# Performance work log

Measured on AMD Instinct MI355X. Metric: run time of the kernel, lower is better.

Reference implementation:

```python
import jax, jax.numpy as jnp
import numpy as np

N, E, IN_CH, EDGE_DIM, N_GRAPHS = 8000, 64000, 256, 16, 64
HEADS = (3, 2, 2, 1)
OUT_CH = (512, 512, 256, 256)
IN_CHS = (IN_CH, 1536, 1024, 512)
NEG_SLOPE = 0.2  # PyG GATv2Conv default negative_slope


def setup_inputs() -> dict:
    key = jax.random.key(0)
    ks = iter(jax.random.split(key, 64))
    d = {}
    d["x"] = jax.random.normal(next(ks), (N, IN_CH), jnp.float32)
    d["edge_index"] = jax.random.randint(next(ks), (2, E), 0, N, dtype=jnp.int32)
    d["edge_attr"] = jax.random.normal(next(ks), (E, EDGE_DIM), jnp.float32)
    d["batch"] = jnp.sort(jax.random.randint(next(ks), (N,), 0, N_GRAPHS, dtype=jnp.int32))
    for i, (ci, h, co) in enumerate(zip(IN_CHS, HEADS, OUT_CH), 1):
        hc = h * co
        s = 1.0 / np.sqrt(ci)
        d[f"W{i}l"] = (jax.random.normal(next(ks), (ci, hc)) * s).astype(jnp.float32)
        d[f"b{i}l"] = jnp.zeros((hc,), jnp.float32)
        d[f"W{i}r"] = (jax.random.normal(next(ks), (ci, hc)) * s).astype(jnp.float32)
        d[f"b{i}r"] = jnp.zeros((hc,), jnp.float32)
        d[f"W{i}e"] = (jax.random.normal(next(ks), (EDGE_DIM, hc)) / np.sqrt(EDGE_DIM)).astype(jnp.float32)
        d[f"att{i}"] = (jax.random.normal(next(ks), (h, co)) / np.sqrt(co)).astype(jnp.float32)
        d[f"bias{i}"] = jnp.zeros((hc,), jnp.float32)
    d["fc1_w"] = (jax.random.normal(next(ks), (256, 64)) / 16.0).astype(jnp.float32)
    d["fc1_b"] = jnp.zeros((64,), jnp.float32)
    d["fc2_w"] = (jax.random.normal(next(ks), (64, 1)) / 8.0).astype(jnp.float32)
    d["fc2_b"] = jnp.zeros((1,), jnp.float32)
    return d


def gatv2(x, src, dst, ea, Wl, bl, Wr, br, We, att, bias, heads, co):
    """GATv2Conv forward (PyG semantics, self-loops already appended in src/dst/ea)."""
    n = x.shape[0]
    xl = (x @ Wl + bl).reshape(n, heads, co)  # applied to source nodes
    xr = (x @ Wr + br).reshape(n, heads, co)  # applied to target nodes
    ee = (ea @ We).reshape(-1, heads, co)     # edge embedding (no bias in PyG)
    m = xl[src] + xr[dst] + ee                # [E', H, C]
    logits = jnp.einsum('ehc,hc->eh', jax.nn.leaky_relu(m, NEG_SLOPE), att)
    # segmented softmax over incoming edges per destination node
    lmax = jax.ops.segment_max(logits, dst, num_segments=n)
    p = jnp.exp(logits - lmax[dst])
    denom = jax.ops.segment_sum(p, dst, num_segments=n)
    alpha = p / denom[dst]                    # every node has a self-loop -> denom > 0
    out = jax.ops.segment_sum(alpha[:, :, None] * xl[src], dst, num_segments=n)
    return out.reshape(n, heads * co) + bias


def _forward(x, edge_index, edge_attr, batch, params, fc):
    n = x.shape[0]
    src0, dst0 = edge_index[0], edge_index[1]
    # add_self_loops with fill_value='mean': per-destination mean of incoming edge_attr
    ea_sum = jax.ops.segment_sum(edge_attr, dst0, num_segments=n)
    ea_cnt = jax.ops.segment_sum(jnp.ones((edge_attr.shape[0], 1), edge_attr.dtype), dst0, num_segments=n)
    ea_loop = ea_sum / jnp.maximum(ea_cnt, 1.0)
    loop = jnp.arange(n, dtype=edge_index.dtype)
    src = jnp.concatenate([src0, loop])
    dst = jnp.concatenate([dst0, loop])
    ea = jnp.concatenate([edge_attr, ea_loop])
    h = x
    for p, hds, co in zip(params, HEADS, OUT_CH):
        h = jax.nn.relu(gatv2(h, src, dst, ea, *p, hds, co))
    # global mean pool over graphs
    s = jax.ops.segment_sum(h, batch, num_segments=N_GRAPHS)
    cnt = jax.ops.segment_sum(jnp.ones((n, 1), h.dtype), batch, num_segments=N_GRAPHS)
    g = s / jnp.maximum(cnt, 1.0)
    # dropout is identity in eval mode
    fc1_w, fc1_b, fc2_w, fc2_b = fc
    g = jax.nn.relu(g @ fc1_w + fc1_b)
    return g @ fc2_w + fc2_b


def reference(x, edge_index, edge_attr, batch,
              W1l, b1l, W1r, b1r, W1e, att1, bias1,
              W2l, b2l, W2r, b2r, W2e, att2, bias2,
              W3l, b3l, W3r, b3r, W3e, att3, bias3,
              W4l, b4l, W4r, b4r, W4e, att4, bias4,
              fc1_w, fc1_b, fc2_w, fc2_b):
    params = [(W1l, b1l, W1r, b1r, W1e, att1, bias1),
              (W2l, b2l, W2r, b2r, W2e, att2, bias2),
              (W3l, b3l, W3r, b3r, W3e, att3, bias3),
              (W4l, b4l, W4r, b4r, W4e, att4, bias4)]
    return _forward(x, edge_index, edge_attr, batch, params, (fc1_w, fc1_b, fc2_w, fc2_b))
```

## Files before the change

### kernel.cpp

```cpp
#include <hip/hip_runtime.h>
#include <math.h>

#define N_NODES 8000
#define N_EDGES 64000
#define ETOT    (N_EDGES + N_NODES)
#define EDIM    16
#define NGRAPHS 64

typedef __attribute__((ext_vector_type(8))) short short8v;
typedef __attribute__((ext_vector_type(4))) short short4v;
typedef __attribute__((ext_vector_type(4))) float f32x4;

__device__ inline unsigned short f2bf(float f) {
    unsigned u = __builtin_bit_cast(unsigned, f);
    unsigned r = (u + 0x7FFF + ((u >> 16) & 1)) >> 16;
    return (unsigned short)r;
}
__device__ inline float bf2f(unsigned short b) {
    unsigned u = ((unsigned)b) << 16;
    return __builtin_bit_cast(float, u);
}

__device__ inline void gload16(const void* g, void* l) {
    __builtin_amdgcn_global_load_lds(
        (const __attribute__((address_space(1))) void*)g,
        (__attribute__((address_space(3))) void*)l, 16, 0, 0);
}


__global__ void count_deg(const int* __restrict__ dst0, int* __restrict__ deg) {
    int e = blockIdx.x * 256 + threadIdx.x;
    if (e < N_EDGES) atomicAdd(&deg[dst0[e]], 1);
}

__global__ void scan_deg2(const int* __restrict__ deg, int* __restrict__ rowptr,
                          int* __restrict__ woff) {
    __shared__ int stot[256];
    int t = threadIdx.x;
    int base = t * 32;
    int sum = 0;
    for (int j = 0; j < 32; j++) {
        int i = base + j;
        if (i < N_NODES) sum += deg[i] + 1;
    }
    stot[t] = sum;
    __syncthreads();
    for (int off = 1; off < 256; off <<= 1) {
        int u = (t >= off) ? stot[t - off] : 0;
        __syncthreads();
        stot[t] += u;
        __syncthreads();
    }
    int run = (t == 0) ? 0 : stot[t - 1];
    if (t == 0) rowptr[0] = 0;
    for (int j = 0; j < 32; j++) {
        int i = base + j;
        if (i < N_NODES) {
            int v = deg[i] + 1;
            woff[i] = run;
            rowptr[i + 1] = run + v;
            run += v;
        }
    }
}

__global__ void fill_eid(const int* __restrict__ dst0, int* __restrict__ woff,
                         int* __restrict__ eid) {
    int i = blockIdx.x * 256 + threadIdx.x;
    if (i < N_EDGES) {
        int pos = atomicAdd(&woff[dst0[i]], 1);
        eid[pos] = i;
    } else if (i < ETOT) {
        int n = i - N_EDGES;
        int pos = atomicAdd(&woff[n], 1);
        eid[pos] = i;
    }
}

__global__ void csr_fill_dst(const int* __restrict__ rowptr, int* __restrict__ csr_dst) {
    int n = blockIdx.x * 256 + threadIdx.x;
    if (n >= N_NODES) return;
    int b = rowptr[n], t = rowptr[n + 1];
    for (int i = b; i < t; i++) csr_dst[i] = n;
}

__global__ void ea_loop_kernel(const int* __restrict__ rowptr, const int* __restrict__ eid,
                               const float* __restrict__ edge_attr, float* __restrict__ ea_loop) {
    int n = blockIdx.x * 256 + threadIdx.x;
    if (n >= N_NODES) return;
    float s[EDIM];
#pragma unroll
    for (int k = 0; k < EDIM; k++) s[k] = 0.f;
    int cnt = 0;
    int b = rowptr[n], t = rowptr[n + 1];
    for (int i = b; i < t; i++) {
        int e = eid[i];
        if (e < N_EDGES) {
            cnt++;
            const float* ea = edge_attr + (size_t)e * EDIM;
#pragma unroll
            for (int k = 0; k < EDIM; k++) s[k] += ea[k];
        }
    }
    float inv = 1.f / (float)(cnt > 0 ? cnt : 1);
#pragma unroll
    for (int k = 0; k < EDIM; k++) ea_loop[(size_t)n * EDIM + k] = s[k] * inv;
}

__global__ void csr_srcea_bf(const int* __restrict__ eid, const int* __restrict__ src0,
                             const float* __restrict__ edge_attr, const float* __restrict__ ea_loop,
                             int* __restrict__ csr_src,
                             short* __restrict__ eah, short* __restrict__ eal) {
    int t = blockIdx.x * 256 + threadIdx.x;
    int i = t >> 2, q = t & 3;
    if (i >= ETOT) return;
    int e = eid[i];
    int s = (e < N_EDGES) ? src0[e] : (e - N_EDGES);
    if (q == 0) csr_src[i] = s;
    const float* ea = (e < N_EDGES) ? edge_attr + (size_t)e * EDIM
                                    : ea_loop + (size_t)(e - N_EDGES) * EDIM;
    float4 v = *(const float4*)(ea + q * 4);
    unsigned short h0 = f2bf(v.x), h1 = f2bf(v.y), h2 = f2bf(v.z), h3 = f2bf(v.w);
    short4v hv = { (short)h0, (short)h1, (short)h2, (short)h3 };
    short4v lv = { (short)f2bf(v.x - bf2f(h0)), (short)f2bf(v.y - bf2f(h1)),
                   (short)f2bf(v.z - bf2f(h2)), (short)f2bf(v.w - bf2f(h3)) };
    short4v zv = { 0, 0, 0, 0 };
    *(short4v*)(eah + (size_t)i * 32 + q * 4) = hv;
    *(short4v*)(eal + (size_t)i * 32 + q * 4) = lv;
    *(short4v*)(eah + (size_t)i * 32 + 16 + q * 4) = zv;
    *(short4v*)(eal + (size_t)i * 32 + 16 + q * 4) = zv;
}

__global__ void cvt_we_all(const float* __restrict__ We1, const float* __restrict__ We2,
                           const float* __restrict__ We3, const float* __restrict__ We4,
                           short* __restrict__ weTh, short* __restrict__ weTl) {
    int ch = blockIdx.x * 256 + threadIdx.x;
    if (ch >= 3328) return;
    const float* We; int lch, hc;
    if (ch < 1536)      { We = We1; lch = ch;        hc = 1536; }
    else if (ch < 2560) { We = We2; lch = ch - 1536; hc = 1024; }
    else if (ch < 3072) { We = We3; lch = ch - 2560; hc = 512;  }
    else                { We = We4; lch = ch - 3072; hc = 256;  }
#pragma unroll
    for (int k = 0; k < EDIM; k++) {
        float v = We[(size_t)k * hc + lch];
        unsigned short h = f2bf(v);
        unsigned short l = f2bf(v - bf2f(h));
        weTh[(size_t)ch * 32 + k] = (short)h;
        weTl[(size_t)ch * 32 + k] = (short)l;
    }
#pragma unroll
    for (int k = EDIM; k < 32; k++) {
        weTh[(size_t)ch * 32 + k] = 0;
        weTl[(size_t)ch * 32 + k] = 0;
    }
}


__global__ __launch_bounds__(256) void cvt_wt_t2(
        const float* __restrict__ Wl, const float* __restrict__ Wr,
        short* __restrict__ WTh, short* __restrict__ WTl, int K, int Nc) {
    __shared__ float sh[32][33];
    const float* W = blockIdx.z ? Wr : Wl;
    size_t obase = blockIdx.z ? (size_t)Nc * K : 0;
    int t = threadIdx.x;
    int tx = t & 31, ty = t >> 5;
    int n0 = blockIdx.x * 32, k0 = blockIdx.y * 32;
#pragma unroll
    for (int j = 0; j < 4; j++)
        sh[ty + j * 8][tx] = W[(size_t)(k0 + ty + j * 8) * Nc + n0 + tx];
    __syncthreads();
#pragma unroll
    for (int j = 0; j < 4; j++) {
        int row = ty + j * 8;
        float v = sh[tx][row];
        unsigned short h = f2bf(v);
        unsigned short l = f2bf(v - bf2f(h));
        size_t idx = obase + (size_t)(n0 + row) * K + k0 + tx;
        WTh[idx] = (short)h;
        WTl[idx] = (short)l;
    }
}


__global__ __launch_bounds__(256) void cvt_act(
        const float* __restrict__ in, short* __restrict__ acth, short* __restrict__ actl,
        int total ) {
    int i = blockIdx.x * 256 + threadIdx.x;
    if (i * 4 >= total) return;
    float4 v = *(const float4*)(in + (size_t)i * 4);
    unsigned short h0 = f2bf(v.x), h1 = f2bf(v.y), h2 = f2bf(v.z), h3 = f2bf(v.w);
    short4v hv = { (short)h0, (short)h1, (short)h2, (short)h3 };
    short4v lv = { (short)f2bf(v.x - bf2f(h0)), (short)f2bf(v.y - bf2f(h1)),
                   (short)f2bf(v.z - bf2f(h2)), (short)f2bf(v.w - bf2f(h3)) };
    *(short4v*)(acth + (size_t)i * 4) = hv;
    *(short4v*)(actl + (size_t)i * 4) = lv;
}


__global__ __launch_bounds__(256) void gemm_mfma3(
        const short* __restrict__ Ah_g, const short* __restrict__ Al_g,
        const short* __restrict__ BTh, const short* __restrict__ BTl,
        const float* __restrict__ bias1, const float* __restrict__ bias2, int hsplit,
        float* __restrict__ C, int M, int K, int Nc) {
    __shared__ __align__(16) short lds[4 * 128 * 32];
    int t = threadIdx.x;
    int m0 = blockIdx.y * 128, n0 = blockIdx.x * 128;
    int lane = t & 63, wave = t >> 6;
    int wm = (wave >> 1) * 64, wn = (wave & 1) * 64;
    int fr = lane & 15, quad = lane >> 4;

    int rl = lane >> 2, seg = lane & 3;
    int perm = seg ^ ((rl >> 1) & 3);
    const short* gp = (wave == 0) ? Ah_g : (wave == 1) ? Al_g : (wave == 2) ? BTh : BTl;
    int brow = (wave < 2) ? m0 : n0;
    const short* src = gp + (size_t)(brow + rl) * K + perm * 8;
    short* ldsw = &lds[wave * 4096];

    int ks = (quad ^ ((fr >> 1) & 3)) << 3;

    f32x4 acc[4][4];
#pragma unroll
    for (int i = 0; i < 4; i++)
#pragma unroll
        for (int j = 0; j < 4; j++) acc[i][j] = (f32x4)(0.f);

    for (int k0 = 0; k0 < K; k0 += 32) {
        __syncthreads();
#pragma unroll
        for (int g = 0; g < 8; g++)
            gload16(src + k0 + (size_t)g * 16 * K, ldsw + g * 512);
        __syncthreads();

        short8v ah[4], al[4], bh[4], bl[4];
#pragma unroll
        for (int mi = 0; mi < 4; mi++) {
            int r = (wm + mi * 16 + fr) * 32 + ks;
            ah[mi] = *(short8v*)&lds[r];
            al[mi] = *(short8v*)&lds[4096 + r];
        }
#pragma unroll
        for (int ni = 0; ni < 4; ni++) {
            int r = (wn + ni * 16 + fr) * 32 + ks;
            bh[ni] = *(short8v*)&lds[8192 + r];
            bl[ni] = *(short8v*)&lds[12288 + r];
        }
#pragma unroll
        for (int mi = 0; mi < 4; mi++)
#pragma unroll
            for (int ni = 0; ni < 4; ni++) {
                acc[mi][ni] = __builtin_amdgcn_mfma_f32_16x16x32_bf16(
                    al[mi], bh[ni], acc[mi][ni], 0, 0, 0);
                acc[mi][ni] = __builtin_amdgcn_mfma_f32_16x16x32_bf16(
                    ah[mi], bl[ni], acc[mi][ni], 0, 0, 0);
                acc[mi][ni] = __builtin_amdgcn_mfma_f32_16x16x32_bf16(
                    ah[mi], bh[ni], acc[mi][ni], 0, 0, 0);
            }
    }

    int rbase = (lane >> 4) * 4;
#pragma unroll
    for (int ni = 0; ni < 4; ni++) {
        int col = n0 + wn + ni * 16 + fr;
        const float* bp = (col < hsplit) ? bias1 + col : bias2 + (col - hsplit);
        float bz = *bp;
#pragma unroll
        for (int mi = 0; mi < 4; mi++) {
            int row0 = m0 + wm + mi * 16 + rbase;
#pragma unroll
            for (int r = 0; r < 4; r++) {
                int row = row0 + r;
                if (row < M) C[(size_t)row * Nc + col] = acc[mi][ni][r] + bz;
            }
        }
    }
}


__global__ __launch_bounds__(256, 4) void edge_logits7(
        const float* __restrict__ xl, const float* __restrict__ xr,
        const short* __restrict__ weTh, const short* __restrict__ weTl,
        const float* __restrict__ att,
        const short* __restrict__ eah, const short* __restrict__ eal,
        const int* __restrict__ csr_src, const int* __restrict__ csr_dst,
        float* __restrict__ logits, int H, int co, int stride) {
    int tid = threadIdx.x;
    int lane = tid & 63, wave = tid >> 6;
    int head = blockIdx.y;
    int cbase = head * co;
    int e0 = blockIdx.x * 64 + wave * 16;
    int col = lane & 15;
    int quad = lane >> 4;
    int e = e0 + col;
    int s = csr_src[e], d = csr_dst[e];
    int ch0 = cbase + quad * 4;

    short8v bh = *(const short8v*)(eah + (size_t)e * 32 + quad * 8);
    short8v bl = *(const short8v*)(eal + (size_t)e * 32 + quad * 8);

    const float* xls = xl + (size_t)s * stride + ch0;
    const float* xrd = xr + (size_t)d * stride + ch0;
    const float* atp = att + ch0;
    const short* wph = weTh + (size_t)(cbase + col) * 32 + quad * 8;
    const short* wpl = weTl + (size_t)(cbase + col) * 32 + quad * 8;

    int ntile = co >> 4;
    float p = 0.f;

    short8v ahA = *(const short8v*)wph;
    short8v alA = *(const short8v*)wpl;
    float4 lvA = *(const float4*)xls;
    float4 rvA = *(const float4*)xrd;
    float4 avA = *(const float4*)atp;

    for (int tt = 0; tt < ntile - 1; tt++) {
        short8v ahB = *(const short8v*)(wph + (size_t)(tt + 1) * 512);
        short8v alB = *(const short8v*)(wpl + (size_t)(tt + 1) * 512);
        float4 lvB = *(const float4*)(xls + (tt + 1) * 16);
        float4 rvB = *(const float4*)(xrd + (tt + 1) * 16);
        float4 avB = *(const float4*)(atp + (tt + 1) * 16);

        f32x4 ee = (f32x4)(0.f);
        ee = __builtin_amdgcn_mfma_f32_16x16x32_bf16(ahA, bl, ee, 0, 0, 0);
        ee = __builtin_amdgcn_mfma_f32_16x16x32_bf16(alA, bh, ee, 0, 0, 0);
        ee = __builtin_amdgcn_mfma_f32_16x16x32_bf16(ahA, bh, ee, 0, 0, 0);
        float m0 = lvA.x + rvA.x + ee[0];
        float m1 = lvA.y + rvA.y + ee[1];
        float m2 = lvA.z + rvA.z + ee[2];
        float m3 = lvA.w + rvA.w + ee[3];
        m0 = (m0 > 0.f) ? m0 : 0.2f * m0;
        m1 = (m1 > 0.f) ? m1 : 0.2f * m1;
        m2 = (m2 > 0.f) ? m2 : 0.2f * m2;
        m3 = (m3 > 0.f) ? m3 : 0.2f * m3;
        p += m0 * avA.x + m1 * avA.y + m2 * avA.z + m3 * avA.w;

        ahA = ahB; alA = alB; lvA = lvB; rvA = rvB; avA = avB;
    }
    {
        f32x4 ee = (f32x4)(0.f);
        ee = __builtin_amdgcn_mfma_f32_16x16x32_bf16(ahA, bl, ee, 0, 0, 0);
        ee = __builtin_amdgcn_mfma_f32_16x16x32_bf16(alA, bh, ee, 0, 0, 0);
        ee = __builtin_amdgcn_mfma_f32_16x16x32_bf16(ahA, bh, ee, 0, 0, 0);
        float m0 = lvA.x + rvA.x + ee[0];
        float m1 = lvA.y + rvA.y + ee[1];
        float m2 = lvA.z + rvA.z + ee[2];
        float m3 = lvA.w + rvA.w + ee[3];
        m0 = (m0 > 0.f) ? m0 : 0.2f * m0;
        m1 = (m1 > 0.f) ? m1 : 0.2f * m1;
        m2 = (m2 > 0.f) ? m2 : 0.2f * m2;
        m3 = (m3 > 0.f) ? m3 : 0.2f * m3;
        p += m0 * avA.x + m1 * avA.y + m2 * avA.z + m3 * avA.w;
    }

    p += __shfl_down(p, 32, 64);
    p += __shfl_down(p, 16, 64);
    if (lane < 16)
        logits[(size_t)(e0 + lane) * H + head] = p;
}


__global__ __launch_bounds__(256) void aggregate5(
        const int* __restrict__ rowptr, const int* __restrict__ csr_src,
        const float* __restrict__ logits, const float* __restrict__ xl,
        const float* __restrict__ bias,
        short* __restrict__ outh, short* __restrict__ outl,
        float* __restrict__ outf, int last,
        int H, int co_shift, int hc, int stride) {
    __shared__ int ssrc[64];
    __shared__ float salp[64][4];
    __shared__ float sm[4], sinv[4];
    int n = blockIdx.x;
    int b = rowptr[n], t = rowptr[n + 1];
    int tid = threadIdx.x;
    int nthr = blockDim.x;

    if (tid < H) {
        float m = -1e30f;
        for (int i = b; i < t; i++)
            m = fmaxf(m, logits[(size_t)i * H + tid]);
        float s = 0.f;
        for (int i = b; i < t; i++)
            s += expf(logits[(size_t)i * H + tid] - m);
        sm[tid] = m;
        sinv[tid] = 1.f / s;
    }
    __syncthreads();

    int j0 = tid * 4;
    int j1 = j0 + nthr * 4;
    int h0 = j0 >> co_shift;
    int h1 = j1 >> co_shift;
    bool act1 = j1 < hc;

    float4 acc0 = make_float4(0.f, 0.f, 0.f, 0.f);
    float4 acc1 = make_float4(0.f, 0.f, 0.f, 0.f);

    for (int cb = b; cb < t; cb += 64) {
        int m = min(64, t - cb);
        __syncthreads();
        for (int i = tid; i < m; i += nthr) {
            ssrc[i] = csr_src[cb + i];
            for (int h = 0; h < H; h++)
                salp[i][h] = expf(logits[(size_t)(cb + i) * H + h] - sm[h]) * sinv[h];
        }
        __syncthreads();
        for (int i = 0; i < m; i++) {
            int s = ssrc[i];
            const float* base = xl + (size_t)s * stride;
            {
                float a = salp[i][h0];
                float4 v = *(const float4*)(base + j0);
                acc0.x += a * v.x; acc0.y += a * v.y;
                acc0.z += a * v.z; acc0.w += a * v.w;
            }
            if (act1) {
                float a = salp[i][h1];
                float4 v = *(const float4*)(base + j1);
                acc1.x += a * v.x; acc1.y += a * v.y;
                acc1.z += a * v.z; acc1.w += a * v.w;
            }
        }
    }

    float4 bz0 = *(const float4*)(bias + j0);
    float4 o0;
    o0.x = fmaxf(acc0.x + bz0.x, 0.f); o0.y = fmaxf(acc0.y + bz0.y, 0.f);
    o0.z = fmaxf(acc0.z + bz0.z, 0.f); o0.w = fmaxf(acc0.w + bz0.w, 0.f);
    if (last) {
        *(float4*)(outf + (size_t)n * hc + j0) = o0;
    } else {
        unsigned short hx = f2bf(o0.x), hy = f2bf(o0.y), hz = f2bf(o0.z), hw = f2bf(o0.w);
        short4v hv = { (short)hx, (short)hy, (short)hz, (short)hw };
        short4v lv = { (short)f2bf(o0.x - bf2f(hx)), (short)f2bf(o0.y - bf2f(hy)),
                       (short)f2bf(o0.z - bf2f(hz)), (short)f2bf(o0.w - bf2f(hw)) };
        *(short4v*)(outh + (size_t)n * hc + j0) = hv;
        *(short4v*)(outl + (size_t)n * hc + j0) = lv;
    }
    if (act1) {
        float4 bz1 = *(const float4*)(bias + j1);
        float4 o1;
        o1.x = fmaxf(acc1.x + bz1.x, 0.f); o1.y = fmaxf(acc1.y + bz1.y, 0.f);
        o1.z = fmaxf(acc1.z + bz1.z, 0.f); o1.w = fmaxf(acc1.w + bz1.w, 0.f);
        if (last) {
            *(float4*)(outf + (size_t)n * hc + j1) = o1;
        } else {
            unsigned short hx = f2bf(o1.x), hy = f2bf(o1.y), hz = f2bf(o1.z), hw = f2bf(o1.w);
            short4v hv = { (short)hx, (short)hy, (short)hz, (short)hw };
            short4v lv = { (short)f2bf(o1.x - bf2f(hx)), (short)f2bf(o1.y - bf2f(hy)),
                           (short)f2bf(o1.z - bf2f(hz)), (short)f2bf(o1.w - bf2f(hw)) };
            *(short4v*)(outh + (size_t)n * hc + j1) = hv;
            *(short4v*)(outl + (size_t)n * hc + j1) = lv;
        }
    }
}


__global__ void pool_cnt(const int* __restrict__ batch, int* __restrict__ gcnt) {
    int n = blockIdx.x * 256 + threadIdx.x;
    if (n < N_NODES) atomicAdd(&gcnt[batch[n]], 1);
}

__global__ void pool_sum(const int* __restrict__ batch, const float* __restrict__ h,
                         float* __restrict__ pooled) {
    int tid = blockIdx.x * 256 + threadIdx.x;
    if (tid >= N_NODES * 256) return;
    int n = tid >> 8, c = tid & 255;
    atomicAdd(&pooled[batch[n] * 256 + c], h[tid]);
}

__global__ void mlp_head(const float* __restrict__ pooled, const int* __restrict__ gcnt,
                         const float* __restrict__ fc1w, const float* __restrict__ fc1b,
                         const float* __restrict__ fc2w, const float* __restrict__ fc2b,
                         float* __restrict__ out) {
    int g = threadIdx.x;
    if (g >= NGRAPHS) return;
    float inv = 1.f / (float)(gcnt[g] > 0 ? gcnt[g] : 1);
    float s[64];
#pragma unroll
    for (int j = 0; j < 64; j++) s[j] = fc1b[j];
    for (int c = 0; c < 256; c++) {
        float mv = pooled[g * 256 + c] * inv;
#pragma unroll
        for (int j = 0; j < 64; j++) s[j] += mv * fc1w[c * 64 + j];
    }
    float o = 0.f;
#pragma unroll
    for (int j = 0; j < 64; j++) o += fmaxf(s[j], 0.f) * fc2w[j];
    out[g] = o + fc2b[0];
}


extern "C" void kernel_launch(void* const* d_in, const int* in_sizes, int n_in,
                              void* d_out, int out_size, void* d_ws, size_t ws_size,
                              hipStream_t stream) {
    const float* x         = (const float*)d_in[0];
    const int*   edge_index= (const int*)d_in[1];
    const float* edge_attr = (const float*)d_in[2];
    const int*   batch     = (const int*)d_in[3];
    const int* src0 = edge_index;
    const int* dst0 = edge_index + N_EDGES;

    const float *Wl[4], *bl[4], *Wr[4], *br[4], *We[4], *att[4], *bias[4];
    for (int i = 0; i < 4; i++) {
        int base = 4 + 7 * i;
        Wl[i]   = (const float*)d_in[base + 0];
        bl[i]   = (const float*)d_in[base + 1];
        Wr[i]   = (const float*)d_in[base + 2];
        br[i]   = (const float*)d_in[base + 3];
        We[i]   = (const float*)d_in[base + 4];
        att[i]  = (const float*)d_in[base + 5];
        bias[i] = (const float*)d_in[base + 6];
    }
    const float* fc1w = (const float*)d_in[32];
    const float* fc1b = (const float*)d_in[33];
    const float* fc2w = (const float*)d_in[34];
    const float* fc2b = (const float*)d_in[35];
    float* out = (float*)d_out;

    float* ws = (float*)d_ws;
    int*   rowptr  = (int*)(ws + 0);
    int*   woff    = (int*)(ws + 8064);
    int*   eid     = (int*)(ws + 16128);
    int*   csr_src = (int*)(ws + 88128);
    int*   csr_dst = (int*)(ws + 160128);
    float* ea_loop = ws + 232128;
    short* weTh_a  = (short*)(ws + 360128);
    short* weTl_a  = (short*)(ws + 413376);
    float* logits  = ws + 1512128;
    float* xlr     = ws + 1728128;
    float* hbF     = xlr + 24576000;
    float* pooled  = hbF + 12288000;
    int*   gcnt    = (int*)(pooled + 16384);
    short* wth     = (short*)(ws + 38608640);
    short* wtl     = (short*)(ws + 40181504);
    short* eah     = (short*)(ws + 41754368);
    short* eal     = (short*)(ws + 42906368);
    short* acth    = (short*)(ws + 44107520);
    short* actl    = (short*)(ws + 50300672);

    hipMemsetAsync(woff, 0, N_NODES * sizeof(int), stream);
    count_deg<<<(N_EDGES + 255) / 256, 256, 0, stream>>>(dst0, woff);
    scan_deg2<<<1, 256, 0, stream>>>(woff, rowptr, woff);
    fill_eid<<<(ETOT + 255) / 256, 256, 0, stream>>>(dst0, woff, eid);
    csr_fill_dst<<<(N_NODES + 255) / 256, 256, 0, stream>>>(rowptr, csr_dst);
    ea_loop_kernel<<<(N_NODES + 255) / 256, 256, 0, stream>>>(rowptr, eid, edge_attr, ea_loop);
    csr_srcea_bf<<<(ETOT * 4 + 255) / 256, 256, 0, stream>>>(eid, src0, edge_attr, ea_loop,
                                                             csr_src, eah, eal);
    cvt_we_all<<<(3328 + 255) / 256, 256, 0, stream>>>(We[0], We[1], We[2], We[3],
                                                       weTh_a, weTl_a);
    cvt_act<<<(N_NODES * 256 / 4 + 255) / 256, 256, 0, stream>>>(x, acth, actl, N_NODES * 256);

    const int IN[4] = {256, 1536, 1024, 512};
    const int HH[4] = {3, 2, 2, 1};
    const int CO[4] = {512, 512, 256, 256};
    const int CS[4] = {9, 9, 8, 8};
    const int CHOFF[4] = {0, 1536, 2560, 3072};

    for (int L = 0; L < 4; L++) {
        int K = IN[L], H = HH[L], co = CO[L], hc = H * co, cs = CS[L];
        int hc2 = 2 * hc;
        dim3 gg(hc2 / 128, (N_NODES + 127) / 128);
        dim3 gw(hc / 32, K / 32, 2);
        cvt_wt_t2<<<gw, 256, 0, stream>>>(Wl[L], Wr[L], wth, wtl, K, hc);
        gemm_mfma3<<<gg, 256, 0, stream>>>(acth, actl, wth, wtl,
                                           bl[L], br[L], hc, xlr, N_NODES, K, hc2);
        dim3 gl(ETOT / 64, H);
        edge_logits7<<<gl, 256, 0, stream>>>(
            xlr, xlr + hc,
            weTh_a + (size_t)CHOFF[L] * 32, weTl_a + (size_t)CHOFF[L] * 32,
            att[L], eah, eal, csr_src, csr_dst, logits, H, co, hc2);
        int athr = hc / 4 > 256 ? 256 : hc / 4;
        aggregate5<<<N_NODES, athr, 0, stream>>>(
            rowptr, csr_src, logits, xlr, bias[L],
            acth, actl, hbF, (L == 3) ? 1 : 0, H, cs, hc, hc2);
    }

    hipMemsetAsync(pooled, 0, (16384 + 64) * sizeof(float), stream);
    pool_cnt<<<(N_NODES + 255) / 256, 256, 0, stream>>>(batch, gcnt);
    pool_sum<<<(N_NODES * 256 + 255) / 256, 256, 0, stream>>>(batch, hbF, pooled);
    mlp_head<<<1, 64, 0, stream>>>(pooled, gcnt, fc1w, fc1b, fc2w, fc2b, out);
}
```

Before: 1.172 ms.

## Double-buffer LDS tiles in split-bf16 MFMA GEMM to overlap loads with compute

Converts the GEMM main loop to a two-stage LDS ping-pong. The next K-tile's global-to-LDS loads are issued before computing on the current tile, with manual vmcnt waits and raw barriers. This aims to hide global load latency behind the MFMA work. LDS use doubles to 64KB per block, which may reduce occupancy.

After: 1.146 ms. 2.3% less time.

```diff
diff --git a/kernel.cpp b/kernel.cpp
--- a/kernel.cpp
+++ b/kernel.cpp
@@ -198,12 +198,12 @@
 }
 
 
-__global__ __launch_bounds__(256) void gemm_mfma3(
+__global__ __launch_bounds__(256) void gemm_mfma4(
         const short* __restrict__ Ah_g, const short* __restrict__ Al_g,
         const short* __restrict__ BTh, const short* __restrict__ BTl,
         const float* __restrict__ bias1, const float* __restrict__ bias2, int hsplit,
         float* __restrict__ C, int M, int K, int Nc) {
-    __shared__ __align__(16) short lds[4 * 128 * 32];
+    __shared__ __align__(16) short lds[2][4 * 128 * 32];
     int t = threadIdx.x;
     int m0 = blockIdx.y * 128, n0 = blockIdx.x * 128;
     int lane = t & 63, wave = t >> 6;
@@ -215,7 +215,7 @@
     const short* gp = (wave == 0) ? Ah_g : (wave == 1) ? Al_g : (wave == 2) ? BTh : BTl;
     int brow = (wave < 2) ? m0 : n0;
     const short* src = gp + (size_t)(brow + rl) * K + perm * 8;
-    short* ldsw = &lds[wave * 4096];
+    int ldswo = wave * 4096;
 
     int ks = (quad ^ ((fr >> 1) & 3)) << 3;
 
@@ -225,25 +225,42 @@
 #pragma unroll
         for (int j = 0; j < 4; j++) acc[i][j] = (f32x4)(0.f);
 
-    for (int k0 = 0; k0 < K; k0 += 32) {
-        __syncthreads();
+    int nt = K >> 5;
+
+    {
+        short* ldsw = &lds[0][ldswo];
 #pragma unroll
         for (int g = 0; g < 8; g++)
-            gload16(src + k0 + (size_t)g * 16 * K, ldsw + g * 512);
-        __syncthreads();
-
+            gload16(src + (size_t)g * 16 * K, ldsw + g * 512);
+    }
+
+    int cur = 0;
+    for (int tt = 0; tt < nt; tt++) {
+        if (tt + 1 < nt) {
+            short* ldsw = &lds[cur ^ 1][ldswo];
+            const short* s2 = src + ((tt + 1) << 5);
+#pragma unroll
+            for (int g = 0; g < 8; g++)
+                gload16(s2 + (size_t)g * 16 * K, ldsw + g * 512);
+            asm volatile("s_waitcnt vmcnt(8)" ::: "memory");
+        } else {
+            asm volatile("s_waitcnt vmcnt(0)" ::: "memory");
+        }
+        __builtin_amdgcn_s_barrier();
+
+        const short* lb = lds[cur];
         short8v ah[4], al[4], bh[4], bl[4];
 #pragma unroll
         for (int mi = 0; mi < 4; mi++) {
             int r = (wm + mi * 16 + fr) * 32 + ks;
-            ah[mi] = *(short8v*)&lds[r];
-            al[mi] = *(short8v*)&lds[4096 + r];
+            ah[mi] = *(const short8v*)&lb[r];
+            al[mi] = *(const short8v*)&lb[4096 + r];
         }
 #pragma unroll
         for (int ni = 0; ni < 4; ni++) {
             int r = (wn + ni * 16 + fr) * 32 + ks;
-            bh[ni] = *(short8v*)&lds[8192 + r];
-            bl[ni] = *(short8v*)&lds[12288 + r];
+            bh[ni] = *(const short8v*)&lb[8192 + r];
+            bl[ni] = *(const short8v*)&lb[12288 + r];
         }
 #pragma unroll
         for (int mi = 0; mi < 4; mi++)
@@ -256,6 +273,10 @@
                 acc[mi][ni] = __builtin_amdgcn_mfma_f32_16x16x32_bf16(
                     ah[mi], bh[ni], acc[mi][ni], 0, 0, 0);
             }
+
+        asm volatile("s_waitcnt lgkmcnt(0)" ::: "memory");
+        __builtin_amdgcn_s_barrier();
+        cur ^= 1;
     }
 
     int rbase = (lane >> 4) * 4;
@@ -562,7 +583,7 @@
         dim3 gg(hc2 / 128, (N_NODES + 127) / 128);
         dim3 gw(hc / 32, K / 32, 2);
         cvt_wt_t2<<<gw, 256, 0, stream>>>(Wl[L], Wr[L], wth, wtl, K, hc);
-        gemm_mfma3<<<gg, 256, 0, stream>>>(acth, actl, wth, wtl,
+        gemm_mfma4<<<gg, 256, 0, stream>>>(acth, actl, wth, wtl,
                                            bl[L], br[L], hc, xlr, N_NODES, K, hc2);
         dim3 gl(ETOT / 64, H);
         edge_logits7<<<gl, 256, 0, stream>>>(
```
